# Performance work log

Hardware: AMD Instinct MI355X
Metric: run time of the kernel (lower is better)

## Reference

```python
import jax, jax.numpy as jnp
import numpy as np

N_NODES = 100000
N_EDGES = 3200000
D_IN = 128
D_HID = 128
N_CLASSES = 64
EPS = 0.0  # GINConv default


def setup_inputs() -> dict:
    key = jax.random.key(0)
    k1, k2, k3, k4, k5, k6 = jax.random.split(key, 6)
    x = jax.random.normal(k1, (N_NODES, D_IN), dtype=jnp.float32)
    edge_index = jax.random.randint(k2, (2, N_EDGES), 0, N_NODES, dtype=jnp.int64)
    s1 = 1.0 / np.sqrt(D_IN)
    W1 = jax.random.uniform(k3, (D_HID, D_IN), minval=-s1, maxval=s1, dtype=jnp.float32)
    b1 = jax.random.uniform(k4, (D_HID,), minval=-s1, maxval=s1, dtype=jnp.float32)
    s2 = 1.0 / np.sqrt(D_HID)
    W2 = jax.random.uniform(k5, (N_CLASSES, D_HID), minval=-s2, maxval=s2, dtype=jnp.float32)
    b2 = jax.random.uniform(k6, (N_CLASSES,), minval=-s2, maxval=s2, dtype=jnp.float32)
    return {"x": x, "edge_index": edge_index, "W1": W1, "b1": b1, "W2": W2, "b2": b2}


def gin_conv(h, src, dst, W, b):
    # sum_{j in N(i)} h_j  : scatter-add of source features into target nodes
    msgs = jnp.take(h, src, axis=0)                       # [E, D]
    agg = jax.ops.segment_sum(msgs, dst, num_segments=N_NODES)  # [N, D]
    z = (1.0 + EPS) * h + agg
    return z @ W.T + b


def reference(x, edge_index, W1, b1, W2, b2):
    src = edge_index[0]
    dst = edge_index[1]
    h = gin_conv(x, src, dst, W1, b1)
    h = jax.nn.relu(h)
    # dropout p=0.5 is identity in eval mode
    out = gin_conv(h, src, dst, W2, b2)
    return out
```

## Files before the change

kernel.cpp:

```cpp
#include <hip/hip_runtime.h>
#include <stdint.h>

#define NN 100000
#define NE 3200000
#define NBK 391
#define NB  500
#define CH  6400
#define CSRCAP 8960
#define GEMM1_BLOCKS 782

typedef unsigned int uint;
typedef unsigned short ushort;
typedef __attribute__((ext_vector_type(8))) short bf16x8;
typedef __attribute__((ext_vector_type(4))) float f32x4;

static __device__ __forceinline__ float bflo(uint v) {
    uint u = v << 16; return __builtin_bit_cast(float, u);
}
static __device__ __forceinline__ float bfhi(uint v) {
    uint u = v & 0xffff0000u; return __builtin_bit_cast(float, u);
}
static __device__ __forceinline__ float bfraw(uint v) {
    return __builtin_bit_cast(float, v);
}
static __device__ __forceinline__ ushort f2b(float f) {
    uint u = __builtin_bit_cast(uint, f);
    u += 0x7fffu + ((u >> 16) & 1u);
    return (ushort)(u >> 16);
}
static __device__ __forceinline__ int wscan(int v, int lane) {
#pragma unroll
    for (int off = 1; off < 64; off <<= 1) {
        int t = __shfl_up(v, off);
        if (lane >= off) v += t;
    }
    return v;
}

__global__ __launch_bounds__(256) void gemm1h_k(const float* __restrict__ x,
                                                const float* __restrict__ W1,
                                                ushort* __restrict__ y1a,
                                                ushort* __restrict__ y1b,
                                                const int* __restrict__ ei,
                                                int* __restrict__ hist) {
    int tid = threadIdx.x;
    if (blockIdx.x >= GEMM1_BLOCKS) {
        __shared__ int hl[NBK];
        int b = blockIdx.x - GEMM1_BLOCKS;
        for (int k = tid; k < NBK; k += 256) hl[k] = 0;
        __syncthreads();
        const int4* dst4 = (const int4*)(ei + NE + b * CH);
        for (int i = tid; i < CH / 4; i += 256) {
            int4 d = dst4[i];
            atomicAdd(&hl[d.x >> 8], 1);
            atomicAdd(&hl[d.y >> 8], 1);
            atomicAdd(&hl[d.z >> 8], 1);
            atomicAdd(&hl[d.w >> 8], 1);
        }
        __syncthreads();
        for (int k = tid; k < NBK; k += 256) hist[b * NBK + k] = hl[k];
        return;
    }

    __shared__ ushort wl[128 * 136];
    for (int i = tid; i < 128 * 128; i += 256)
        wl[(i >> 7) * 136 + (i & 127)] = f2b(W1[i]);
    __syncthreads();

    int wave = tid >> 6, lane = tid & 63;
    int lr = lane & 15, lk = (lane >> 4) * 8;
    long rowbase = (long)blockIdx.x * 128 + wave * 32;

    f32x4 acc[2][8] = {};
    for (int kc = 0; kc < 128; kc += 32) {
        bf16x8 a[2];
#pragma unroll
        for (int m = 0; m < 2; m++) {
            long row = rowbase + m * 16 + lr;
            if (row > NN - 1) row = NN - 1;
            const float* p = x + row * 128 + kc + lk;
            float f[8];
            *(float4*)(f)     = *(const float4*)(p);
            *(float4*)(f + 4) = *(const float4*)(p + 4);
            bf16x8 t;
#pragma unroll
            for (int j = 0; j < 8; j++) t[j] = (short)f2b(f[j]);
            a[m] = t;
        }
#pragma unroll
        for (int nb = 0; nb < 8; nb++) {
            bf16x8 b = *(const bf16x8*)&wl[(nb * 16 + lr) * 136 + kc + lk];
            acc[0][nb] = __builtin_amdgcn_mfma_f32_16x16x32_bf16(a[0], b, acc[0][nb], 0, 0, 0);
            acc[1][nb] = __builtin_amdgcn_mfma_f32_16x16x32_bf16(a[1], b, acc[1][nb], 0, 0, 0);
        }
    }
    int rq = (lane >> 4) * 4;
#pragma unroll
    for (int m = 0; m < 2; m++) {
#pragma unroll
        for (int r = 0; r < 4; r++) {
            long row = rowbase + m * 16 + rq + r;
            if (row < NN) {
#pragma unroll
                for (int nb = 0; nb < 8; nb++) {
                    ushort v = f2b(acc[m][nb][r]);
                    if (nb < 4) y1a[row * 64 + nb * 16 + lr] = v;
                    else        y1b[row * 64 + (nb - 4) * 16 + lr] = v;
                }
            }
        }
    }
}

__global__ __launch_bounds__(64) void pbase_k(const int* __restrict__ hist,
                                              int* __restrict__ pbase,
                                              int* __restrict__ totals) {
    int k = blockIdx.x, lane = threadIdx.x;
    int carry = 0;
#pragma unroll
    for (int c = 0; c < 8; ++c) {
        int b = c * 64 + lane;
        int v = (b < NB) ? hist[b * NBK + k] : 0;
        int incl = wscan(v, lane);
        if (b < NB) pbase[b * NBK + k] = carry + incl - v;
        carry += __shfl(incl, 63);
    }
    if (lane == 0) totals[k] = carry;
}

__global__ __launch_bounds__(1024) void bscan_k(const int* __restrict__ totals,
                                                int* __restrict__ gbase,
                                                int* __restrict__ nodeptr,
                                                ushort* __restrict__ y1a,
                                                ushort* __restrict__ y1b,
                                                ushort* __restrict__ y2) {
    __shared__ int sd[1024];
    int t = threadIdx.x;
    int v = (t < NBK) ? totals[t] : 0;
    sd[t] = v;
    __syncthreads();
    for (int off = 1; off < 1024; off <<= 1) {
        int u = (t >= off) ? sd[t - off] : 0;
        __syncthreads();
        sd[t] += u;
        __syncthreads();
    }
    int excl = sd[t] - v;
    if (t < NBK) gbase[t] = excl;
    if (t == 0) { gbase[NBK] = NE; nodeptr[NN] = NE; }
    if (t < 32)              ((uint*)(y1a + (size_t)NN * 64))[t] = 0;
    else if (t < 64)         ((uint*)(y1b + (size_t)NN * 64))[t - 32] = 0;
    else if (t < 96)         ((uint*)(y2  + (size_t)NN * 64))[t - 64] = 0;
}

__global__ __launch_bounds__(512) void bfill2_k(const int* __restrict__ ei,
                                                const int* __restrict__ pbase,
                                                const int* __restrict__ gbase,
                                                uint* __restrict__ barr) {
    __shared__ int cur[NBK];
    int tid = threadIdx.x, b = blockIdx.x;
    for (int k = tid; k < NBK; k += 512)
        cur[k] = gbase[k] + pbase[b * NBK + k];
    __syncthreads();
    const int4* src4 = (const int4*)(ei + b * CH);
    const int4* dst4 = (const int4*)(ei + NE + b * CH);
    for (int i = tid; i < CH / 4; i += 512) {
        int4 s = src4[i];
        int4 d = dst4[i];
        int p0 = atomicAdd(&cur[d.x >> 8], 1);
        barr[p0] = ((uint)(d.x & 255) << 17) | (uint)s.x;
        int p1 = atomicAdd(&cur[d.y >> 8], 1);
        barr[p1] = ((uint)(d.y & 255) << 17) | (uint)s.y;
        int p2 = atomicAdd(&cur[d.z >> 8], 1);
        barr[p2] = ((uint)(d.z & 255) << 17) | (uint)s.z;
        int p3 = atomicAdd(&cur[d.w >> 8], 1);
        barr[p3] = ((uint)(d.w & 255) << 17) | (uint)s.w;
    }
}

__global__ __launch_bounds__(256) void csr_k(const uint* __restrict__ barr,
                                             const int* __restrict__ gbase,
                                             int* __restrict__ nodeptr,
                                             uint* __restrict__ col) {
    __shared__ uint stg[CSRCAP];
    __shared__ int cnt[256], cur[256];
    int tid = threadIdx.x;
    int blk = blockIdx.x;
    int s0 = gbase[blk], s1 = gbase[blk + 1];
    int n = s1 - s0;
    bool fits = (n <= CSRCAP);
    cnt[tid] = 0;
    __syncthreads();
    if (fits) {
        for (int i = tid; i < n; i += 256) {
            uint e = barr[s0 + i];
            stg[i] = e;
            atomicAdd(&cnt[e >> 17], 1);
        }
    } else {
        for (int i = s0 + tid; i < s1; i += 256)
            atomicAdd(&cnt[barr[i] >> 17], 1);
    }
    __syncthreads();
    if (tid < 64) {
        int c0 = cnt[4 * tid], c1 = cnt[4 * tid + 1];
        int c2 = cnt[4 * tid + 2], c3 = cnt[4 * tid + 3];
        int s = c0 + c1 + c2 + c3;
        int incl = wscan(s, tid);
        int excl = incl - s;
        cur[4 * tid]     = excl;
        cur[4 * tid + 1] = excl + c0;
        cur[4 * tid + 2] = excl + c0 + c1;
        cur[4 * tid + 3] = excl + c0 + c1 + c2;
        int node = blk * 256 + 4 * tid;
        if (node < NN)     nodeptr[node]     = s0 + excl;
        if (node + 1 < NN) nodeptr[node + 1] = s0 + excl + c0;
        if (node + 2 < NN) nodeptr[node + 2] = s0 + excl + c0 + c1;
        if (node + 3 < NN) nodeptr[node + 3] = s0 + excl + c0 + c1 + c2;
    }
    __syncthreads();
    if (fits) {
        for (int i = tid; i < n; i += 256) {
            uint e = stg[i];
            int pos = s0 + atomicAdd(&cur[e >> 17], 1);
            col[pos] = e & 0x1FFFF;
        }
    } else {
        for (int i = s0 + tid; i < s1; i += 256) {
            uint e = barr[i];
            int pos = s0 + atomicAdd(&cur[e >> 17], 1);
            col[pos] = e & 0x1FFFF;
        }
    }
}

__global__ __launch_bounds__(256) void gemm2_k(const ushort* __restrict__ ha,
                                               const ushort* __restrict__ hb,
                                               const float* __restrict__ W2,
                                               ushort* __restrict__ y2) {
    __shared__ ushort wl[64 * 136];
    int tid = threadIdx.x;
    for (int i = tid; i < 64 * 128; i += 256)
        wl[(i >> 7) * 136 + (i & 127)] = f2b(W2[i]);
    __syncthreads();

    int wave = tid >> 6, lane = tid & 63;
    int lr = lane & 15, lk = (lane >> 4) * 8;
    long rowbase = (long)blockIdx.x * 128 + wave * 32;

    f32x4 acc[2][4] = {};
#pragma unroll
    for (int kc = 0; kc < 128; kc += 32) {
        const ushort* hsrc = (kc < 64) ? ha : hb;
        int koff = kc & 63;
        bf16x8 a[2];
#pragma unroll
        for (int m = 0; m < 2; m++) {
            long row = rowbase + m * 16 + lr;
            if (row > NN - 1) row = NN - 1;
            a[m] = *(const bf16x8*)(hsrc + row * 64 + koff + lk);
        }
#pragma unroll
        for (int nb = 0; nb < 4; nb++) {
            bf16x8 b = *(const bf16x8*)&wl[(nb * 16 + lr) * 136 + kc + lk];
            acc[0][nb] = __builtin_amdgcn_mfma_f32_16x16x32_bf16(a[0], b, acc[0][nb], 0, 0, 0);
            acc[1][nb] = __builtin_amdgcn_mfma_f32_16x16x32_bf16(a[1], b, acc[1][nb], 0, 0, 0);
        }
    }
    int rq = (lane >> 4) * 4;
#pragma unroll
    for (int m = 0; m < 2; m++) {
#pragma unroll
        for (int r = 0; r < 4; r++) {
            long row = rowbase + m * 16 + rq + r;
            if (row < NN) {
#pragma unroll
                for (int nb = 0; nb < 4; nb++)
                    y2[row * 64 + nb * 16 + lr] = f2b(acc[m][nb][r]);
            }
        }
    }
}


__global__ __launch_bounds__(256) void agg1h_k(const ushort* __restrict__ yh,
                                               const int* __restrict__ nodeptr,
                                               const uint* __restrict__ col,
                                               const float* __restrict__ bh,
                                               ushort* __restrict__ hh) {
    int wid = (blockIdx.x * 256 + threadIdx.x) >> 6;
    int lane = threadIdx.x & 63;
    if (wid >= NN) return;
    int s0 = nodeptr[wid], s1 = nodeptr[wid + 1];
    int o = lane >> 3, r = lane & 7;

    float aLo[4] = {}, aHi[4] = {};
    const ushort* yr = yh + r * 8;

    for (int i = s0; i < s1; i += 64) {
        int m = s1 - i; if (m > 64) m = 64;
        int sv = (lane < m) ? (int)col[i + lane] : NN;
        int jg = (m + 31) >> 5;
        for (int g = 0; g < jg; ++g) {
            int e0 = 32 * g + o;
            int sj0 = __shfl(sv, e0);
            int sj1 = __shfl(sv, e0 + 8);
            int sj2 = __shfl(sv, e0 + 16);
            int sj3 = __shfl(sv, e0 + 24);
            uint4 u0 = *(const uint4*)(yr + (size_t)sj0 * 64);
            uint4 u1 = *(const uint4*)(yr + (size_t)sj1 * 64);
            uint4 u2 = *(const uint4*)(yr + (size_t)sj2 * 64);
            uint4 u3 = *(const uint4*)(yr + (size_t)sj3 * 64);
            aLo[0] += bflo(u0.x); aHi[0] += bfraw(u0.x);
            aLo[1] += bflo(u0.y); aHi[1] += bfraw(u0.y);
            aLo[2] += bflo(u0.z); aHi[2] += bfraw(u0.z);
            aLo[3] += bflo(u0.w); aHi[3] += bfraw(u0.w);
            aLo[0] += bflo(u1.x); aHi[0] += bfraw(u1.x);
            aLo[1] += bflo(u1.y); aHi[1] += bfraw(u1.y);
            aLo[2] += bflo(u1.z); aHi[2] += bfraw(u1.z);
            aLo[3] += bflo(u1.w); aHi[3] += bfraw(u1.w);
            aLo[0] += bflo(u2.x); aHi[0] += bfraw(u2.x);
            aLo[1] += bflo(u2.y); aHi[1] += bfraw(u2.y);
            aLo[2] += bflo(u2.z); aHi[2] += bfraw(u2.z);
            aLo[3] += bflo(u2.w); aHi[3] += bfraw(u2.w);
            aLo[0] += bflo(u3.x); aHi[0] += bfraw(u3.x);
            aLo[1] += bflo(u3.y); aHi[1] += bfraw(u3.y);
            aLo[2] += bflo(u3.z); aHi[2] += bfraw(u3.z);
            aLo[3] += bflo(u3.w); aHi[3] += bfraw(u3.w);
        }
    }
#pragma unroll
    for (int d = 0; d < 4; ++d) {
        aLo[d] += __shfl_xor(aLo[d], 8);  aHi[d] += __shfl_xor(aHi[d], 8);
        aLo[d] += __shfl_xor(aLo[d], 16); aHi[d] += __shfl_xor(aHi[d], 16);
        aLo[d] += __shfl_xor(aLo[d], 32); aHi[d] += __shfl_xor(aHi[d], 32);
    }
    if (o == 0) {
        uint4 s = *(const uint4*)(yh + (size_t)wid * 64 + r * 8);
        float4 bA = *(const float4*)(bh + r * 8);
        float4 bB = *(const float4*)(bh + r * 8 + 4);
        float v0 = fmaxf(aLo[0] + bflo(s.x) + bA.x, 0.f);
        float v1 = fmaxf(aHi[0] + bfhi(s.x) + bA.y, 0.f);
        float v2 = fmaxf(aLo[1] + bflo(s.y) + bA.z, 0.f);
        float v3 = fmaxf(aHi[1] + bfhi(s.y) + bA.w, 0.f);
        float v4 = fmaxf(aLo[2] + bflo(s.z) + bB.x, 0.f);
        float v5 = fmaxf(aHi[2] + bfhi(s.z) + bB.y, 0.f);
        float v6 = fmaxf(aLo[3] + bflo(s.w) + bB.z, 0.f);
        float v7 = fmaxf(aHi[3] + bfhi(s.w) + bB.w, 0.f);
        uint4 out;
        out.x = (uint)f2b(v0) | ((uint)f2b(v1) << 16);
        out.y = (uint)f2b(v2) | ((uint)f2b(v3) << 16);
        out.z = (uint)f2b(v4) | ((uint)f2b(v5) << 16);
        out.w = (uint)f2b(v6) | ((uint)f2b(v7) << 16);
        *(uint4*)(hh + (size_t)wid * 64 + r * 8) = out;
    }
}

__global__ __launch_bounds__(256) void agg2_k(const ushort* __restrict__ y2,
                                              const int* __restrict__ nodeptr,
                                              const uint* __restrict__ col,
                                              const float* __restrict__ b2,
                                              float* __restrict__ out) {
    int wid = (blockIdx.x * 256 + threadIdx.x) >> 6;
    int lane = threadIdx.x & 63;
    if (wid >= NN) return;
    int s0 = nodeptr[wid], s1 = nodeptr[wid + 1];
    int o = lane >> 3, r = lane & 7;

    float aLo[4] = {}, aHi[4] = {};
    const ushort* yr = y2 + r * 8;

    for (int i = s0; i < s1; i += 64) {
        int m = s1 - i; if (m > 64) m = 64;
        int sv = (lane < m) ? (int)col[i + lane] : NN;
        int jg = (m + 31) >> 5;
        for (int g = 0; g < jg; ++g) {
            int e0 = 32 * g + o;
            int sj0 = __shfl(sv, e0);
            int sj1 = __shfl(sv, e0 + 8);
            int sj2 = __shfl(sv, e0 + 16);
            int sj3 = __shfl(sv, e0 + 24);
            uint4 u0 = *(const uint4*)(yr + (size_t)sj0 * 64);
            uint4 u1 = *(const uint4*)(yr + (size_t)sj1 * 64);
            uint4 u2 = *(const uint4*)(yr + (size_t)sj2 * 64);
            uint4 u3 = *(const uint4*)(yr + (size_t)sj3 * 64);
            aLo[0] += bflo(u0.x); aHi[0] += bfraw(u0.x);
            aLo[1] += bflo(u0.y); aHi[1] += bfraw(u0.y);
            aLo[2] += bflo(u0.z); aHi[2] += bfraw(u0.z);
            aLo[3] += bflo(u0.w); aHi[3] += bfraw(u0.w);
            aLo[0] += bflo(u1.x); aHi[0] += bfraw(u1.x);
            aLo[1] += bflo(u1.y); aHi[1] += bfraw(u1.y);
            aLo[2] += bflo(u1.z); aHi[2] += bfraw(u1.z);
            aLo[3] += bflo(u1.w); aHi[3] += bfraw(u1.w);
            aLo[0] += bflo(u2.x); aHi[0] += bfraw(u2.x);
            aLo[1] += bflo(u2.y); aHi[1] += bfraw(u2.y);
            aLo[2] += bflo(u2.z); aHi[2] += bfraw(u2.z);
            aLo[3] += bflo(u2.w); aHi[3] += bfraw(u2.w);
            aLo[0] += bflo(u3.x); aHi[0] += bfraw(u3.x);
            aLo[1] += bflo(u3.y); aHi[1] += bfraw(u3.y);
            aLo[2] += bflo(u3.z); aHi[2] += bfraw(u3.z);
            aLo[3] += bflo(u3.w); aHi[3] += bfraw(u3.w);
        }
    }
#pragma unroll
    for (int d = 0; d < 4; ++d) {
        aLo[d] += __shfl_xor(aLo[d], 8);  aHi[d] += __shfl_xor(aHi[d], 8);
        aLo[d] += __shfl_xor(aLo[d], 16); aHi[d] += __shfl_xor(aHi[d], 16);
        aLo[d] += __shfl_xor(aLo[d], 32); aHi[d] += __shfl_xor(aHi[d], 32);
    }
    if (o == 0) {
        uint4 s = *(const uint4*)(y2 + (size_t)wid * 64 + r * 8);
        float4 bA = *(const float4*)(b2 + r * 8);
        float4 bB = *(const float4*)(b2 + r * 8 + 4);
        float4 o0, o1;
        o0.x = aLo[0] + bflo(s.x) + bA.x;
        o0.y = aHi[0] + bfhi(s.x) + bA.y;
        o0.z = aLo[1] + bflo(s.y) + bA.z;
        o0.w = aHi[1] + bfhi(s.y) + bA.w;
        o1.x = aLo[2] + bflo(s.z) + bB.x;
        o1.y = aHi[2] + bfhi(s.z) + bB.y;
        o1.z = aLo[3] + bflo(s.w) + bB.z;
        o1.w = aHi[3] + bfhi(s.w) + bB.w;
        *(float4*)(out + (size_t)wid * 64 + r * 8)     = o0;
        *(float4*)(out + (size_t)wid * 64 + r * 8 + 4) = o1;
    }
}


static constexpr size_t alup(size_t x) { return (x + 255) & ~(size_t)255; }
static constexpr size_t OFF_HIST  = 0;
static constexpr size_t OFF_PBASE = alup(OFF_HIST  + (size_t)NB * NBK * 4);
static constexpr size_t OFF_TOT   = alup(OFF_PBASE + (size_t)NB * NBK * 4);
static constexpr size_t OFF_GBASE = alup(OFF_TOT   + NBK * 4);
static constexpr size_t OFF_NPTR  = alup(OFF_GBASE + (NBK + 1) * 4);
static constexpr size_t OFF_BARR  = alup(OFF_NPTR  + (size_t)(NN + 1) * 4);
static constexpr size_t OFF_COL   = alup(OFF_BARR  + (size_t)NE * 4);
static constexpr size_t OFF_Y1A   = alup(OFF_COL   + (size_t)NE * 4);
static constexpr size_t OFF_Y1B   = alup(OFF_Y1A + (size_t)(NN + 1) * 64 * 2);
static constexpr size_t OFF_HA    = alup(OFF_Y1B + (size_t)(NN + 1) * 64 * 2);
static constexpr size_t OFF_HB    = alup(OFF_HA  + (size_t)(NN + 1) * 64 * 2);
static constexpr size_t OFF_Y2    = alup(OFF_HB  + (size_t)(NN + 1) * 64 * 2);

extern "C" void kernel_launch(void* const* d_in, const int* in_sizes, int n_in,
                              void* d_out, int out_size, void* d_ws, size_t ws_size,
                              hipStream_t stream) {
    const float* x  = (const float*)d_in[0];
    const int*   ei = (const int*)d_in[1];
    const float* W1 = (const float*)d_in[2];
    const float* b1 = (const float*)d_in[3];
    const float* W2 = (const float*)d_in[4];
    const float* b2 = (const float*)d_in[5];
    float* out = (float*)d_out;
    char* ws = (char*)d_ws;

    int*  hist  = (int*)(ws + OFF_HIST);
    int*  pbase = (int*)(ws + OFF_PBASE);
    int*  tot   = (int*)(ws + OFF_TOT);
    int*  gbase = (int*)(ws + OFF_GBASE);
    int*  nptr  = (int*)(ws + OFF_NPTR);
    uint* barr  = (uint*)(ws + OFF_BARR);
    uint* colA  = (uint*)(ws + OFF_COL);
    ushort* y1a = (ushort*)(ws + OFF_Y1A);
    ushort* y1b = (ushort*)(ws + OFF_Y1B);
    ushort* ha  = (ushort*)(ws + OFF_HA);
    ushort* hb  = (ushort*)(ws + OFF_HB);
    ushort* y2  = (ushort*)(ws + OFF_Y2);

    hipLaunchKernelGGL(gemm1h_k, dim3(GEMM1_BLOCKS + NB), dim3(256), 0, stream,
                       x, W1, y1a, y1b, ei, hist);
    hipLaunchKernelGGL(pbase_k,  dim3(NBK), dim3(64),   0, stream, hist, pbase, tot);
    hipLaunchKernelGGL(bscan_k,  dim3(1),   dim3(1024), 0, stream, tot, gbase, nptr, y1a, y1b, y2);
    hipLaunchKernelGGL(bfill2_k, dim3(NB),  dim3(512),  0, stream, ei, pbase, gbase, barr);
    hipLaunchKernelGGL(csr_k,    dim3(NBK), dim3(256),  0, stream, barr, gbase, nptr, colA);

    hipLaunchKernelGGL(agg1h_k, dim3(25000),dim3(256), 0, stream, y1a, nptr, colA, b1,      ha);
    hipLaunchKernelGGL(agg1h_k, dim3(25000),dim3(256), 0, stream, y1b, nptr, colA, b1 + 64, hb);
    hipLaunchKernelGGL(gemm2_k, dim3(782),  dim3(256), 0, stream, ha, hb, W2, y2);
    hipLaunchKernelGGL(agg2_k,  dim3(25000),dim3(256), 0, stream, y2, nptr, colA, b2, out);
}
```

Measured before the change: 242.6 us.

## Store projected node features as FP8 and merge the two layer-1 aggregation passes

New measurement: 226.3 us. 6.7% less time.

```diff
diff --git a/kernel.cpp b/kernel.cpp
--- a/kernel.cpp
+++ b/kernel.cpp
@@ -11,23 +11,26 @@
 
 typedef unsigned int uint;
 typedef unsigned short ushort;
+typedef unsigned char uchar;
 typedef __attribute__((ext_vector_type(8))) short bf16x8;
 typedef __attribute__((ext_vector_type(4))) float f32x4;
+typedef __attribute__((ext_vector_type(2))) float f32x2;
 
 static __device__ __forceinline__ float bflo(uint v) {
     uint u = v << 16; return __builtin_bit_cast(float, u);
 }
 static __device__ __forceinline__ float bfhi(uint v) {
     uint u = v & 0xffff0000u; return __builtin_bit_cast(float, u);
-}
-static __device__ __forceinline__ float bfraw(uint v) {
-    return __builtin_bit_cast(float, v);
 }
 static __device__ __forceinline__ ushort f2b(float f) {
     uint u = __builtin_bit_cast(uint, f);
     u += 0x7fffu + ((u >> 16) & 1u);
     return (ushort)(u >> 16);
 }
+static __device__ __forceinline__ uchar f2e(float f) {
+    int e = __builtin_amdgcn_cvt_pk_fp8_f32(f, 0.f, 0, false);
+    return (uchar)(e & 0xff);
+}
 static __device__ __forceinline__ int wscan(int v, int lane) {
 #pragma unroll
     for (int off = 1; off < 64; off <<= 1) {
@@ -37,10 +40,15 @@
     return v;
 }
 
+#define DEC4(W, A0, A1, A2, A3)                                           \
+    { f32x2 p_ = __builtin_amdgcn_cvt_pk_f32_fp8((int)(W), false);        \
+      A0 += p_.x; A1 += p_.y;                                             \
+      p_ = __builtin_amdgcn_cvt_pk_f32_fp8((int)(W), true);               \
+      A2 += p_.x; A3 += p_.y; }
+
 __global__ __launch_bounds__(256) void gemm1h_k(const float* __restrict__ x,
                                                 const float* __restrict__ W1,
-                                                ushort* __restrict__ y1a,
-                                                ushort* __restrict__ y1b,
+                                                uchar* __restrict__ y1,
                                                 const int* __restrict__ ei,
                                                 int* __restrict__ hist) {
     int tid = threadIdx.x;
@@ -102,11 +110,8 @@
             long row = rowbase + m * 16 + rq + r;
             if (row < NN) {
 #pragma unroll
-                for (int nb = 0; nb < 8; nb++) {
-                    ushort v = f2b(acc[m][nb][r]);
-                    if (nb < 4) y1a[row * 64 + nb * 16 + lr] = v;
-                    else        y1b[row * 64 + (nb - 4) * 16 + lr] = v;
-                }
+                for (int nb = 0; nb < 8; nb++)
+                    y1[row * 128 + nb * 16 + lr] = f2e(acc[m][nb][r]);
             }
         }
     }
@@ -131,9 +136,8 @@
 __global__ __launch_bounds__(1024) void bscan_k(const int* __restrict__ totals,
                                                 int* __restrict__ gbase,
                                                 int* __restrict__ nodeptr,
-                                                ushort* __restrict__ y1a,
-                                                ushort* __restrict__ y1b,
-                                                ushort* __restrict__ y2) {
+                                                uchar* __restrict__ y1,
+                                                uchar* __restrict__ y2) {
     __shared__ int sd[1024];
     int t = threadIdx.x;
     int v = (t < NBK) ? totals[t] : 0;
@@ -148,9 +152,8 @@
     int excl = sd[t] - v;
     if (t < NBK) gbase[t] = excl;
     if (t == 0) { gbase[NBK] = NE; nodeptr[NN] = NE; }
-    if (t < 32)              ((uint*)(y1a + (size_t)NN * 64))[t] = 0;
-    else if (t < 64)         ((uint*)(y1b + (size_t)NN * 64))[t - 32] = 0;
-    else if (t < 96)         ((uint*)(y2  + (size_t)NN * 64))[t - 64] = 0;
+    if (t < 32)              ((uint*)(y1 + (size_t)NN * 128))[t] = 0;
+    else if (t < 48)         ((uint*)(y2 + (size_t)NN * 64))[t - 32] = 0;
 }
 
 __global__ __launch_bounds__(512) void bfill2_k(const int* __restrict__ ei,
@@ -234,10 +237,9 @@
     }
 }
 
-__global__ __launch_bounds__(256) void gemm2_k(const ushort* __restrict__ ha,
-                                               const ushort* __restrict__ hb,
+__global__ __launch_bounds__(256) void gemm2_k(const ushort* __restrict__ h,
                                                const float* __restrict__ W2,
-                                               ushort* __restrict__ y2) {
+                                               uchar* __restrict__ y2) {
     __shared__ ushort wl[64 * 136];
     int tid = threadIdx.x;
     for (int i = tid; i < 64 * 128; i += 256)
@@ -249,16 +251,13 @@
     long rowbase = (long)blockIdx.x * 128 + wave * 32;
 
     f32x4 acc[2][4] = {};
-#pragma unroll
     for (int kc = 0; kc < 128; kc += 32) {
-        const ushort* hsrc = (kc < 64) ? ha : hb;
-        int koff = kc & 63;
         bf16x8 a[2];
 #pragma unroll
         for (int m = 0; m < 2; m++) {
             long row = rowbase + m * 16 + lr;
             if (row > NN - 1) row = NN - 1;
-            a[m] = *(const bf16x8*)(hsrc + row * 64 + koff + lk);
+            a[m] = *(const bf16x8*)(h + row * 128 + kc + lk);
         }
 #pragma unroll
         for (int nb = 0; nb < 4; nb++) {
@@ -276,26 +275,25 @@
             if (row < NN) {
 #pragma unroll
                 for (int nb = 0; nb < 4; nb++)
-                    y2[row * 64 + nb * 16 + lr] = f2b(acc[m][nb][r]);
+                    y2[row * 64 + nb * 16 + lr] = f2e(acc[m][nb][r]);
             }
         }
     }
 }
 
-
-__global__ __launch_bounds__(256) void agg1h_k(const ushort* __restrict__ yh,
+__global__ __launch_bounds__(256) void agg1f_k(const uchar* __restrict__ y1,
                                                const int* __restrict__ nodeptr,
                                                const uint* __restrict__ col,
-                                               const float* __restrict__ bh,
-                                               ushort* __restrict__ hh) {
+                                               const float* __restrict__ b1,
+                                               ushort* __restrict__ h) {
     int wid = (blockIdx.x * 256 + threadIdx.x) >> 6;
     int lane = threadIdx.x & 63;
     if (wid >= NN) return;
     int s0 = nodeptr[wid], s1 = nodeptr[wid + 1];
     int o = lane >> 3, r = lane & 7;
 
-    float aLo[4] = {}, aHi[4] = {};
-    const ushort* yr = yh + r * 8;
+    float acc[16] = {};
+    const uchar* yr = y1 + r * 16;
 
     for (int i = s0; i < s1; i += 64) {
         int m = s1 - i; if (m > 64) m = 64;
@@ -307,68 +305,74 @@
             int sj1 = __shfl(sv, e0 + 8);
             int sj2 = __shfl(sv, e0 + 16);
             int sj3 = __shfl(sv, e0 + 24);
-            uint4 u0 = *(const uint4*)(yr + (size_t)sj0 * 64);
-            uint4 u1 = *(const uint4*)(yr + (size_t)sj1 * 64);
-            uint4 u2 = *(const uint4*)(yr + (size_t)sj2 * 64);
-            uint4 u3 = *(const uint4*)(yr + (size_t)sj3 * 64);
-            aLo[0] += bflo(u0.x); aHi[0] += bfraw(u0.x);
-            aLo[1] += bflo(u0.y); aHi[1] += bfraw(u0.y);
-            aLo[2] += bflo(u0.z); aHi[2] += bfraw(u0.z);
-            aLo[3] += bflo(u0.w); aHi[3] += bfraw(u0.w);
-            aLo[0] += bflo(u1.x); aHi[0] += bfraw(u1.x);
-            aLo[1] += bflo(u1.y); aHi[1] += bfraw(u1.y);
-            aLo[2] += bflo(u1.z); aHi[2] += bfraw(u1.z);
-            aLo[3] += bflo(u1.w); aHi[3] += bfraw(u1.w);
-            aLo[0] += bflo(u2.x); aHi[0] += bfraw(u2.x);
-            aLo[1] += bflo(u2.y); aHi[1] += bfraw(u2.y);
-            aLo[2] += bflo(u2.z); aHi[2] += bfraw(u2.z);
-            aLo[3] += bflo(u2.w); aHi[3] += bfraw(u2.w);
-            aLo[0] += bflo(u3.x); aHi[0] += bfraw(u3.x);
-            aLo[1] += bflo(u3.y); aHi[1] += bfraw(u3.y);
-            aLo[2] += bflo(u3.z); aHi[2] += bfraw(u3.z);
-            aLo[3] += bflo(u3.w); aHi[3] += bfraw(u3.w);
-        }
-    }
-#pragma unroll
-    for (int d = 0; d < 4; ++d) {
-        aLo[d] += __shfl_xor(aLo[d], 8);  aHi[d] += __shfl_xor(aHi[d], 8);
-        aLo[d] += __shfl_xor(aLo[d], 16); aHi[d] += __shfl_xor(aHi[d], 16);
-        aLo[d] += __shfl_xor(aLo[d], 32); aHi[d] += __shfl_xor(aHi[d], 32);
+            uint4 u0 = *(const uint4*)(yr + (size_t)sj0 * 128);
+            uint4 u1 = *(const uint4*)(yr + (size_t)sj1 * 128);
+            uint4 u2 = *(const uint4*)(yr + (size_t)sj2 * 128);
+            uint4 u3 = *(const uint4*)(yr + (size_t)sj3 * 128);
+            DEC4(u0.x, acc[0], acc[1], acc[2], acc[3]);
+            DEC4(u0.y, acc[4], acc[5], acc[6], acc[7]);
+            DEC4(u0.z, acc[8], acc[9], acc[10], acc[11]);
+            DEC4(u0.w, acc[12], acc[13], acc[14], acc[15]);
+            DEC4(u1.x, acc[0], acc[1], acc[2], acc[3]);
+            DEC4(u1.y, acc[4], acc[5], acc[6], acc[7]);
+            DEC4(u1.z, acc[8], acc[9], acc[10], acc[11]);
+            DEC4(u1.w, acc[12], acc[13], acc[14], acc[15]);
+            DEC4(u2.x, acc[0], acc[1], acc[2], acc[3]);
+            DEC4(u2.y, acc[4], acc[5], acc[6], acc[7]);
+            DEC4(u2.z, acc[8], acc[9], acc[10], acc[11]);
+            DEC4(u2.w, acc[12], acc[13], acc[14], acc[15]);
+            DEC4(u3.x, acc[0], acc[1], acc[2], acc[3]);
+            DEC4(u3.y, acc[4], acc[5], acc[6], acc[7]);
+            DEC4(u3.z, acc[8], acc[9], acc[10], acc[11]);
+            DEC4(u3.w, acc[12], acc[13], acc[14], acc[15]);
+        }
+    }
+#pragma unroll
+    for (int d = 0; d < 16; ++d) {
+        acc[d] += __shfl_xor(acc[d], 8);
+        acc[d] += __shfl_xor(acc[d], 16);
+        acc[d] += __shfl_xor(acc[d], 32);
     }
     if (o == 0) {
-        uint4 s = *(const uint4*)(yh + (size_t)wid * 64 + r * 8);
-        float4 bA = *(const float4*)(bh + r * 8);
-        float4 bB = *(const float4*)(bh + r * 8 + 4);
-        float v0 = fmaxf(aLo[0] + bflo(s.x) + bA.x, 0.f);
-        float v1 = fmaxf(aHi[0] + bfhi(s.x) + bA.y, 0.f);
-        float v2 = fmaxf(aLo[1] + bflo(s.y) + bA.z, 0.f);
-        float v3 = fmaxf(aHi[1] + bfhi(s.y) + bA.w, 0.f);
-        float v4 = fmaxf(aLo[2] + bflo(s.z) + bB.x, 0.f);
-        float v5 = fmaxf(aHi[2] + bfhi(s.z) + bB.y, 0.f);
-        float v6 = fmaxf(aLo[3] + bflo(s.w) + bB.z, 0.f);
-        float v7 = fmaxf(aHi[3] + bfhi(s.w) + bB.w, 0.f);
-        uint4 out;
-        out.x = (uint)f2b(v0) | ((uint)f2b(v1) << 16);
-        out.y = (uint)f2b(v2) | ((uint)f2b(v3) << 16);
-        out.z = (uint)f2b(v4) | ((uint)f2b(v5) << 16);
-        out.w = (uint)f2b(v6) | ((uint)f2b(v7) << 16);
-        *(uint4*)(hh + (size_t)wid * 64 + r * 8) = out;
-    }
-}
-
-__global__ __launch_bounds__(256) void agg2_k(const ushort* __restrict__ y2,
-                                              const int* __restrict__ nodeptr,
-                                              const uint* __restrict__ col,
-                                              const float* __restrict__ b2,
-                                              float* __restrict__ out) {
+        uint4 s4 = *(const uint4*)(y1 + (size_t)wid * 128 + r * 16);
+        float sv[16] = {};
+        DEC4(s4.x, sv[0], sv[1], sv[2], sv[3]);
+        DEC4(s4.y, sv[4], sv[5], sv[6], sv[7]);
+        DEC4(s4.z, sv[8], sv[9], sv[10], sv[11]);
+        DEC4(s4.w, sv[12], sv[13], sv[14], sv[15]);
+        const float* bp = b1 + r * 16;
+        float4 b0 = *(const float4*)(bp);
+        float4 b1v = *(const float4*)(bp + 4);
+        float4 b2v = *(const float4*)(bp + 8);
+        float4 b3v = *(const float4*)(bp + 12);
+        float bb[16] = {b0.x, b0.y, b0.z, b0.w, b1v.x, b1v.y, b1v.z, b1v.w,
+                        b2v.x, b2v.y, b2v.z, b2v.w, b3v.x, b3v.y, b3v.z, b3v.w};
+        uint hw[8];
+#pragma unroll
+        for (int j = 0; j < 8; ++j) {
+            float v0 = fmaxf(acc[2 * j] + sv[2 * j] + bb[2 * j], 0.f);
+            float v1 = fmaxf(acc[2 * j + 1] + sv[2 * j + 1] + bb[2 * j + 1], 0.f);
+            hw[j] = (uint)f2b(v0) | ((uint)f2b(v1) << 16);
+        }
+        ushort* hp = h + (size_t)wid * 128 + r * 16;
+        *(uint4*)(hp)     = make_uint4(hw[0], hw[1], hw[2], hw[3]);
+        *(uint4*)(hp + 8) = make_uint4(hw[4], hw[5], hw[6], hw[7]);
+    }
+}
+
+__global__ __launch_bounds__(256) void agg2f_k(const uchar* __restrict__ y2,
+                                               const int* __restrict__ nodeptr,
+                                               const uint* __restrict__ col,
+                                               const float* __restrict__ b2,
+                                               float* __restrict__ out) {
     int wid = (blockIdx.x * 256 + threadIdx.x) >> 6;
     int lane = threadIdx.x & 63;
     if (wid >= NN) return;
     int s0 = nodeptr[wid], s1 = nodeptr[wid + 1];
     int o = lane >> 3, r = lane & 7;
 
-    float aLo[4] = {}, aHi[4] = {};
-    const ushort* yr = y2 + r * 8;
+    float acc[8] = {};
+    const uchar* yr = y2 + r * 8;
 
     for (int i = s0; i < s1; i += 64) {
         int m = s1 - i; if (m > 64) m = 64;
@@ -380,47 +384,43 @@
             int sj1 = __shfl(sv, e0 + 8);
             int sj2 = __shfl(sv, e0 + 16);
             int sj3 = __shfl(sv, e0 + 24);
-            uint4 u0 = *(const uint4*)(yr + (size_t)sj0 * 64);
-            uint4 u1 = *(const uint4*)(yr + (size_t)sj1 * 64);
-            uint4 u2 = *(const uint4*)(yr + (size_t)sj2 * 64);
-            uint4 u3 = *(const uint4*)(yr + (size_t)sj3 * 64);
-            aLo[0] += bflo(u0.x); aHi[0] += bfraw(u0.x);
-            aLo[1] += bflo(u0.y); aHi[1] += bfraw(u0.y);
-            aLo[2] += bflo(u0.z); aHi[2] += bfraw(u0.z);
-            aLo[3] += bflo(u0.w); aHi[3] += bfraw(u0.w);
-            aLo[0] += bflo(u1.x); aHi[0] += bfraw(u1.x);
-            aLo[1] += bflo(u1.y); aHi[1] += bfraw(u1.y);
-            aLo[2] += bflo(u1.z); aHi[2] += bfraw(u1.z);
-            aLo[3] += bflo(u1.w); aHi[3] += bfraw(u1.w);
-            aLo[0] += bflo(u2.x); aHi[0] += bfraw(u2.x);
-            aLo[1] += bflo(u2.y); aHi[1] += bfraw(u2.y);
-            aLo[2] += bflo(u2.z); aHi[2] += bfraw(u2.z);
-            aLo[3] += bflo(u2.w); aHi[3] += bfraw(u2.w);
-            aLo[0] += bflo(u3.x); aHi[0] += bfraw(u3.x);
-            aLo[1] += bflo(u3.y); aHi[1] += bfraw(u3.y);
-            aLo[2] += bflo(u3.z); aHi[2] += bfraw(u3.z);
-            aLo[3] += bflo(u3.w); aHi[3] += bfraw(u3.w);
-        }
-    }
-#pragma unroll
-    for (int d = 0; d < 4; ++d) {
-        aLo[d] += __shfl_xor(aLo[d], 8);  aHi[d] += __shfl_xor(aHi[d], 8);
-        aLo[d] += __shfl_xor(aLo[d], 16); aHi[d] += __shfl_xor(aHi[d], 16);
-        aLo[d] += __shfl_xor(aLo[d], 32); aHi[d] += __shfl_xor(aHi[d], 32);
+            uint2 u0 = *(const uint2*)(yr + (size_t)sj0 * 64);
+            uint2 u1 = *(const uint2*)(yr + (size_t)sj1 * 64);
+            uint2 u2 = *(const uint2*)(yr + (size_t)sj2 * 64);
+            uint2 u3 = *(const uint2*)(yr + (size_t)sj3 * 64);
+            DEC4(u0.x, acc[0], acc[1], acc[2], acc[3]);
+            DEC4(u0.y, acc[4], acc[5], acc[6], acc[7]);
+            DEC4(u1.x, acc[0], acc[1], acc[2], acc[3]);
+            DEC4(u1.y, acc[4], acc[5], acc[6], acc[7]);
+            DEC4(u2.x, acc[0], acc[1], acc[2], acc[3]);
+            DEC4(u2.y, acc[4], acc[5], acc[6], acc[7]);
+            DEC4(u3.x, acc[0], acc[1], acc[2], acc[3]);
+            DEC4(u3.y, acc[4], acc[5], acc[6], acc[7]);
+        }
+    }
+#pragma unroll
+    for (int d = 0; d < 8; ++d) {
+        acc[d] += __shfl_xor(acc[d], 8);
+        acc[d] += __shfl_xor(acc[d], 16);
+        acc[d] += __shfl_xor(acc[d], 32);
     }
     if (o == 0) {
-        uint4 s = *(const uint4*)(y2 + (size_t)wid * 64 + r * 8);
-        float4 bA = *(const float4*)(b2 + r * 8);
-        float4 bB = *(const float4*)(b2 + r * 8 + 4);
+        uint2 s2 = *(const uint2*)(y2 + (size_t)wid * 64 + r * 8);
+        float sv8[8] = {};
+        DEC4(s2.x, sv8[0], sv8[1], sv8[2], sv8[3]);
+        DEC4(s2.y, sv8[4], sv8[5], sv8[6], sv8[7]);
+        const float* bp = b2 + r * 8;
+        float4 bA = *(const float4*)(bp);
+        float4 bB = *(const float4*)(bp + 4);
         float4 o0, o1;
-        o0.x = aLo[0] + bflo(s.x) + bA.x;
-        o0.y = aHi[0] + bfhi(s.x) + bA.y;
-        o0.z = aLo[1] + bflo(s.y) + bA.z;
-        o0.w = aHi[1] + bfhi(s.y) + bA.w;
-        o1.x = aLo[2] + bflo(s.z) + bB.x;
-        o1.y = aHi[2] + bfhi(s.z) + bB.y;
-        o1.z = aLo[3] + bflo(s.w) + bB.z;
-        o1.w = aHi[3] + bfhi(s.w) + bB.w;
+        o0.x = acc[0] + sv8[0] + bA.x;
+        o0.y = acc[1] + sv8[1] + bA.y;
+        o0.z = acc[2] + sv8[2] + bA.z;
+        o0.w = acc[3] + sv8[3] + bA.w;
+        o1.x = acc[4] + sv8[4] + bB.x;
+        o1.y = acc[5] + sv8[5] + bB.y;
+        o1.z = acc[6] + sv8[6] + bB.z;
+        o1.w = acc[7] + sv8[7] + bB.w;
         *(float4*)(out + (size_t)wid * 64 + r * 8)     = o0;
         *(float4*)(out + (size_t)wid * 64 + r * 8 + 4) = o1;
     }
@@ -435,11 +435,9 @@
 static constexpr size_t OFF_NPTR  = alup(OFF_GBASE + (NBK + 1) * 4);
 static constexpr size_t OFF_BARR  = alup(OFF_NPTR  + (size_t)(NN + 1) * 4);
 static constexpr size_t OFF_COL   = alup(OFF_BARR  + (size_t)NE * 4);
-static constexpr size_t OFF_Y1A   = alup(OFF_COL   + (size_t)NE * 4);
-static constexpr size_t OFF_Y1B   = alup(OFF_Y1A + (size_t)(NN + 1) * 64 * 2);
-static constexpr size_t OFF_HA    = alup(OFF_Y1B + (size_t)(NN + 1) * 64 * 2);
-static constexpr size_t OFF_HB    = alup(OFF_HA  + (size_t)(NN + 1) * 64 * 2);
-static constexpr size_t OFF_Y2    = alup(OFF_HB  + (size_t)(NN + 1) * 64 * 2);
+static constexpr size_t OFF_Y1    = alup(OFF_COL   + (size_t)NE * 4);
+static constexpr size_t OFF_H     = alup(OFF_Y1 + (size_t)(NN + 1) * 128);
+static constexpr size_t OFF_Y2    = alup(OFF_H  + (size_t)NN * 128 * 2);
 
 extern "C" void kernel_launch(void* const* d_in, const int* in_sizes, int n_in,
                               void* d_out, int out_size, void* d_ws, size_t ws_size,
@@ -460,21 +458,18 @@
     int*  nptr  = (int*)(ws + OFF_NPTR);
     uint* barr  = (uint*)(ws + OFF_BARR);
     uint* colA  = (uint*)(ws + OFF_COL);
-    ushort* y1a = (ushort*)(ws + OFF_Y1A);
-    ushort* y1b = (ushort*)(ws + OFF_Y1B);
-    ushort* ha  = (ushort*)(ws + OFF_HA);
-    ushort* hb  = (ushort*)(ws + OFF_HB);
-    ushort* y2  = (ushort*)(ws + OFF_Y2);
+    uchar* y1   = (uchar*)(ws + OFF_Y1);
+    ushort* hh  = (ushort*)(ws + OFF_H);
+    uchar* y2   = (uchar*)(ws + OFF_Y2);
 
     hipLaunchKernelGGL(gemm1h_k, dim3(GEMM1_BLOCKS + NB), dim3(256), 0, stream,
-                       x, W1, y1a, y1b, ei, hist);
+                       x, W1, y1, ei, hist);
     hipLaunchKernelGGL(pbase_k,  dim3(NBK), dim3(64),   0, stream, hist, pbase, tot);
-    hipLaunchKernelGGL(bscan_k,  dim3(1),   dim3(1024), 0, stream, tot, gbase, nptr, y1a, y1b, y2);
+    hipLaunchKernelGGL(bscan_k,  dim3(1),   dim3(1024), 0, stream, tot, gbase, nptr, y1, y2);
     hipLaunchKernelGGL(bfill2_k, dim3(NB),  dim3(512),  0, stream, ei, pbase, gbase, barr);
     hipLaunchKernelGGL(csr_k,    dim3(NBK), dim3(256),  0, stream, barr, gbase, nptr, colA);
 
-    hipLaunchKernelGGL(agg1h_k, dim3(25000),dim3(256), 0, stream, y1a, nptr, colA, b1,      ha);
-    hipLaunchKernelGGL(agg1h_k, dim3(25000),dim3(256), 0, stream, y1b, nptr, colA, b1 + 64, hb);
-    hipLaunchKernelGGL(gemm2_k, dim3(782),  dim3(256), 0, stream, ha, hb, W2, y2);
-    hipLaunchKernelGGL(agg2_k,  dim3(25000),dim3(256), 0, stream, y2, nptr, colA, b2, out);
-}
+    hipLaunchKernelGGL(agg1f_k, dim3(25000), dim3(256), 0, stream, y1, nptr, colA, b1, hh);
+    hipLaunchKernelGGL(gemm2_k, dim3(782),   dim3(256), 0, stream, hh, W2, y2);
+    hipLaunchKernelGGL(agg2f_k, dim3(25000), dim3(256), 0, stream, y2, nptr, colA, b2, out);
+}
```
